# Kernel tuning notes

Hardware: AMD Instinct MI355X
Metric: run time of the kernel (lower is better)

Reference implementation:

```python
import jax, jax.numpy as jnp
import numpy as np

B, S, D, H = 4, 2048, 1024, 16
DH = D // H
NEG = -1e9


def setup_inputs() -> dict:
    key = jax.random.key(0)
    ks = jax.random.split(key, 6)
    return {
        "q_raw": jax.random.normal(ks[0], (B, S, D), jnp.float32),
        "kv_raw": jax.random.normal(ks[1], (B, S, D), jnp.float32),
        "padding_mask": jnp.ones((B, S), jnp.int32),
        "Wq": jax.random.normal(ks[2], (D, D), jnp.float32) * 0.02,
        "Wk": jax.random.normal(ks[3], (D, D), jnp.float32) * 0.02,
        "Wv": jax.random.normal(ks[4], (D, D), jnp.float32) * 0.02,
        "Wo": jax.random.normal(ks[5], (D, D), jnp.float32) * 0.02,
    }


def _split_heads(x):
    # (B, S, D) -> (B, H, S, DH)
    return x.reshape(B, S, H, DH).transpose(0, 2, 1, 3)


def reference(q_raw, kv_raw, padding_mask, Wq, Wk, Wv, Wo):
    # nn.Linear (no bias): y = x @ W.T
    q = _split_heads(q_raw @ Wq.T)
    k = _split_heads(kv_raw @ Wk.T)
    v = _split_heads(kv_raw @ Wv.T)

    scale = 1.0 / jnp.sqrt(jnp.float32(DH))
    scores = jnp.einsum("bhqd,bhkd->bhqk", q, k) * scale  # (B,H,S,S)

    # padding mask: 0 -> masked (broadcast over query dim), as in torch code
    pad = (padding_mask == 0)[:, None, None, :]  # (B,1,1,S)
    scores = jnp.where(pad, NEG, scores)
    # causal mask (only applied when padding_mask given, matching original)
    causal = jnp.triu(jnp.ones((S, S), bool), k=1)  # (S,S)
    scores = jnp.where(causal[None, None], NEG, scores)

    w = jax.nn.softmax(scores, axis=-1)
    att = jnp.einsum("bhqk,bhkd->bhqd", w, v)  # (B,H,S,DH)
    att = att.transpose(0, 2, 1, 3).reshape(B, S, D)
    return att @ Wo.T
```

## Files before the change

kernel.cpp:

```cpp
#include <hip/hip_runtime.h>
#include <stdint.h>

typedef __attribute__((ext_vector_type(8))) short  short8;
typedef __attribute__((ext_vector_type(4))) float  f32x4;
typedef __attribute__((ext_vector_type(4))) unsigned short us4;
typedef __attribute__((ext_vector_type(4))) unsigned int u32x4;

static __device__ __forceinline__ unsigned short f2bf(float x) {
  unsigned u = __builtin_bit_cast(unsigned, x);
  u += 0x7FFFu + ((u >> 16) & 1u);
  return (unsigned short)(u >> 16);
}

static __device__ __forceinline__ unsigned cvt_pk_bf16(float lo, float hi) {
  unsigned r;
  asm("v_cvt_pk_bf16_f32 %0, %1, %2" : "=v"(r) : "v"(lo), "v"(hi));
  return r;
}

__global__ __launch_bounds__(256) void cvt6(const float* __restrict__ q_raw,
                                            const float* __restrict__ kv_raw,
                                            const float* __restrict__ Wq,
                                            const float* __restrict__ Wk,
                                            const float* __restrict__ Wv,
                                            const float* __restrict__ Wo,
                                            unsigned short* __restrict__ qbf,
                                            unsigned short* __restrict__ kvbf,
                                            unsigned short* __restrict__ wbf) {
  const int y = blockIdx.y;
  const float* in;
  unsigned short* out;
  int n4;
  if (y == 0)      { in = q_raw;  out = qbf;  n4 = 2097152; }
  else if (y == 1) { in = kv_raw; out = kvbf; n4 = 2097152; }
  else {
    in  = (y == 2) ? Wq : (y == 3) ? Wk : (y == 4) ? Wv : Wo;
    out = wbf + (size_t)(y - 2) * 1048576;
    n4 = 262144;
  }
  int i = blockIdx.x * 256 + threadIdx.x;
  const int stride = gridDim.x * 256;
  for (; i < n4; i += stride) {
    f32x4 v = *((const f32x4*)in + i);
    us4 o = { f2bf(v[0]), f2bf(v[1]), f2bf(v[2]), f2bf(v[3]) };
    *((us4*)out + i) = o;
  }
}

__global__ __launch_bounds__(1024) void bias_kernel(const int* __restrict__ pm,
                                                    float* __restrict__ bias,
                                                    unsigned* __restrict__ flagmask) {
  __shared__ unsigned m;
  const int b = blockIdx.x, tid = threadIdx.x;
  if (tid == 0) m = 0;
  __syncthreads();
  const int i0 = b * 2048 + tid;
  const int z0 = pm[i0], z1 = pm[i0 + 1024];
  bias[i0]        = z0 ? 0.f : -1.0e9f;
  bias[i0 + 1024] = z1 ? 0.f : -1.0e9f;
  const int wv = tid >> 6;
  unsigned long long b0 = __ballot(z0 == 0);
  unsigned long long b1 = __ballot(z1 == 0);
  if ((tid & 63) == 0) {
    unsigned bits = (b0 ? (1u << wv) : 0u) | (b1 ? (1u << (wv + 16)) : 0u);
    if (bits) atomicOr(&m, bits);
  }
  __syncthreads();
  if (tid == 0) flagmask[b] = m;
}

static __device__ __forceinline__ void g2l16(const void* g, void* l) {
  __builtin_amdgcn_global_load_lds(
      (const __attribute__((address_space(1))) void*)g,
      (__attribute__((address_space(3))) void*)l, 16, 0, 0);
}

__global__ __launch_bounds__(256, 5) void gemm_proj(const unsigned short* __restrict__ qbf,
                                                    const unsigned short* __restrict__ kvbf,
                                                    const unsigned short* __restrict__ wbf,
                                                    unsigned short* __restrict__ Qp,
                                                    unsigned short* __restrict__ Kp,
                                                    unsigned short* __restrict__ Vtp,
                                                    float qscale) {
  __shared__ unsigned short Alds[2][4096];
  __shared__ unsigned short Blds[2][4096];
  const int tid  = threadIdx.x;
  const int lane = tid & 63;
  const int w    = tid >> 6;
  const int g    = lane >> 4;
  const int li   = lane & 15;

  const int l = blockIdx.x;
  const int xcd = l & 7, j = l >> 3;
  const int mstep = j & 7, rn = j >> 3;
  const int region = rn >> 3;
  const int n0 = (rn & 7) * 128;
  const int m0 = (xcd * 8 + mstep) * 128;
  const int wm = (w >> 1) * 64;
  const int wn = (w & 1) * 64;

  const unsigned short* A = (region == 0) ? qbf : kvbf;
  const unsigned short* W = wbf + (size_t)region * 1048576;

  int aoff[4], boff[4];
#pragma unroll
  for (int mi = 0; mi < 4; ++mi) {
    int row = wm + mi * 16 + li;
    aoff[mi] = row * 32 + (g ^ ((row >> 1) & 3)) * 8;
  }
#pragma unroll
  for (int ni = 0; ni < 4; ++ni) {
    int col = wn + ni * 16 + li;
    boff[ni] = col * 32 + (g ^ ((col >> 1) & 3)) * 8;
  }

  const int s1 = tid, s2 = 256 + tid;
  const int r1 = s1 >> 2, gc1 = (s1 & 3) ^ ((r1 >> 1) & 3);
  const int r2 = s2 >> 2, gc2 = (s2 & 3) ^ ((r2 >> 1) & 3);
  const unsigned short* gA1 = A + (size_t)(m0 + r1) * 1024 + gc1 * 8;
  const unsigned short* gA2 = A + (size_t)(m0 + r2) * 1024 + gc2 * 8;
  const unsigned short* gB1 = W + (size_t)(n0 + r1) * 1024 + gc1 * 8;
  const unsigned short* gB2 = W + (size_t)(n0 + r2) * 1024 + gc2 * 8;

  f32x4 acc[4][4] = {};

  g2l16(gA1, &Alds[0][w * 512]); g2l16(gA2, &Alds[0][2048 + w * 512]);
  g2l16(gB1, &Blds[0][w * 512]); g2l16(gB2, &Blds[0][2048 + w * 512]);
  gA1 += 32; gA2 += 32; gB1 += 32; gB2 += 32;

  int cur = 0;
#pragma unroll 1
  for (int kt = 0; kt < 32; ++kt) {
    if (kt < 31) {
      g2l16(gA1, &Alds[cur ^ 1][w * 512]); g2l16(gA2, &Alds[cur ^ 1][2048 + w * 512]);
      g2l16(gB1, &Blds[cur ^ 1][w * 512]); g2l16(gB2, &Blds[cur ^ 1][2048 + w * 512]);
      gA1 += 32; gA2 += 32; gB1 += 32; gB2 += 32;
      asm volatile("s_waitcnt vmcnt(4)" ::: "memory");
    } else {
      asm volatile("s_waitcnt vmcnt(0)" ::: "memory");
    }
    __builtin_amdgcn_s_barrier();
    short8 af[4], bf[4];
#pragma unroll
    for (int mi = 0; mi < 4; ++mi) af[mi] = *(const short8*)&Alds[cur][aoff[mi]];
#pragma unroll
    for (int ni = 0; ni < 4; ++ni) bf[ni] = *(const short8*)&Blds[cur][boff[ni]];
#pragma unroll
    for (int mi = 0; mi < 4; ++mi)
#pragma unroll
      for (int ni = 0; ni < 4; ++ni)
        acc[mi][ni] = __builtin_amdgcn_mfma_f32_16x16x32_bf16(af[mi], bf[ni], acc[mi][ni], 0, 0, 0);
    __builtin_amdgcn_s_barrier();
    cur ^= 1;
  }

  if (region == 2) {
#pragma unroll
    for (int mi = 0; mi < 4; ++mi) {
      int mb = m0 + wm + mi * 16 + g * 4;
      int bb = mb >> 11, s = mb & 2047;
#pragma unroll
      for (int ni = 0; ni < 4; ++ni) {
        int n = n0 + wn + ni * 16 + li;
        us4 pk = { f2bf(acc[mi][ni][0]), f2bf(acc[mi][ni][1]),
                   f2bf(acc[mi][ni][2]), f2bf(acc[mi][ni][3]) };
        *(us4*)&Vtp[(size_t)(bb * 1024 + n) * 2048 + s] = pk;
      }
    }
  } else {
    unsigned short* C = (region == 0) ? Qp : Kp;
    const float sc = (region == 0) ? qscale : 1.0f;
#pragma unroll
    for (int mi = 0; mi < 4; ++mi) {
      int mb = m0 + wm + mi * 16 + g * 4;
#pragma unroll
      for (int ni = 0; ni < 4; ++ni) {
        int n = n0 + wn + ni * 16 + li;
#pragma unroll
        for (int r = 0; r < 4; ++r)
          C[(size_t)(mb + r) * 1024 + n] = f2bf(acc[mi][ni][r] * sc);
      }
    }
  }
}

__global__ __launch_bounds__(256) void gemm_out(const unsigned short* __restrict__ A,
                                                const unsigned short* __restrict__ W,
                                                float* __restrict__ C) {
  __shared__ unsigned short Alds[2][4096];
  __shared__ unsigned short Blds[2][4096];
  const int tid  = threadIdx.x;
  const int lane = tid & 63;
  const int w    = tid >> 6;
  const int g    = lane >> 4;
  const int li   = lane & 15;

  const int l = blockIdx.x;
  const int xcd = l & 7, j = l >> 3;
  const int mstep = j & 7, nt = j >> 3;
  const int m0 = (xcd * 8 + mstep) * 128;
  const int n0 = nt * 128;
  const int wm = (w >> 1) * 64;
  const int wn = (w & 1) * 64;

  int aoff[4], boff[4];
#pragma unroll
  for (int mi = 0; mi < 4; ++mi) {
    int row = wm + mi * 16 + li;
    aoff[mi] = row * 32 + (g ^ ((row >> 1) & 3)) * 8;
  }
#pragma unroll
  for (int ni = 0; ni < 4; ++ni) {
    int col = wn + ni * 16 + li;
    boff[ni] = col * 32 + (g ^ ((col >> 1) & 3)) * 8;
  }

  const int s1 = tid, s2 = 256 + tid;
  const int r1 = s1 >> 2, gc1 = (s1 & 3) ^ ((r1 >> 1) & 3);
  const int r2 = s2 >> 2, gc2 = (s2 & 3) ^ ((r2 >> 1) & 3);
  const unsigned short* gA1 = A + (size_t)(m0 + r1) * 1024 + gc1 * 8;
  const unsigned short* gA2 = A + (size_t)(m0 + r2) * 1024 + gc2 * 8;
  const unsigned short* gB1 = W + (size_t)(n0 + r1) * 1024 + gc1 * 8;
  const unsigned short* gB2 = W + (size_t)(n0 + r2) * 1024 + gc2 * 8;

  f32x4 acc[4][4] = {};

  g2l16(gA1, &Alds[0][w * 512]); g2l16(gA2, &Alds[0][2048 + w * 512]);
  g2l16(gB1, &Blds[0][w * 512]); g2l16(gB2, &Blds[0][2048 + w * 512]);
  gA1 += 32; gA2 += 32; gB1 += 32; gB2 += 32;

  int cur = 0;
#pragma unroll 1
  for (int kt = 0; kt < 32; ++kt) {
    if (kt < 31) {
      g2l16(gA1, &Alds[cur ^ 1][w * 512]); g2l16(gA2, &Alds[cur ^ 1][2048 + w * 512]);
      g2l16(gB1, &Blds[cur ^ 1][w * 512]); g2l16(gB2, &Blds[cur ^ 1][2048 + w * 512]);
      gA1 += 32; gA2 += 32; gB1 += 32; gB2 += 32;
      asm volatile("s_waitcnt vmcnt(4)" ::: "memory");
    } else {
      asm volatile("s_waitcnt vmcnt(0)" ::: "memory");
    }
    __builtin_amdgcn_s_barrier();
    short8 af[4], bf[4];
#pragma unroll
    for (int mi = 0; mi < 4; ++mi) af[mi] = *(const short8*)&Alds[cur][aoff[mi]];
#pragma unroll
    for (int ni = 0; ni < 4; ++ni) bf[ni] = *(const short8*)&Blds[cur][boff[ni]];
#pragma unroll
    for (int mi = 0; mi < 4; ++mi)
#pragma unroll
      for (int ni = 0; ni < 4; ++ni)
        acc[mi][ni] = __builtin_amdgcn_mfma_f32_16x16x32_bf16(af[mi], bf[ni], acc[mi][ni], 0, 0, 0);
    __builtin_amdgcn_s_barrier();
    cur ^= 1;
  }

#pragma unroll
  for (int mi = 0; mi < 4; ++mi) {
    int mb = m0 + wm + mi * 16 + g * 4;
#pragma unroll
    for (int ni = 0; ni < 4; ++ni) {
      int n = n0 + wn + ni * 16 + li;
#pragma unroll
      for (int r = 0; r < 4; ++r)
        C[(size_t)(mb + r) * 1024 + n] = acc[mi][ni][r];
    }
  }
}

__global__ __launch_bounds__(256, 4) void attn_kernel(const unsigned short* __restrict__ Qp,
                                                      const unsigned short* __restrict__ Kp,
                                                      const unsigned short* __restrict__ Vt,
                                                      const float* __restrict__ bias,
                                                      const unsigned* __restrict__ flagmask,
                                                      unsigned short* __restrict__ att) {
  __shared__ unsigned short Klds[2][64 * 64];
  __shared__ unsigned short Vlds[2][64 * 64];

  const int tid = threadIdx.x, lane = tid & 63, w = tid >> 6;
  const int g = lane >> 4, li = lane & 15;

  const int rid = blockIdx.x + (blockIdx.y << 4);
  const int xcd = rid & 7, kk = rid >> 3;
  const int bh = (kk & 7) | (xcd << 3);
  const int b = bh >> 4, h = bh & 15;
  const int tA = kk >> 3, tB = 31 - tA;
  const int nA = tA + 1, nB = tB + 1;

  const unsigned smask = flagmask[b];

  const int s1 = tid, s2 = tid + 256;
  const int r1 = s1 >> 3, c1 = (s1 & 7) ^ (r1 & 7);
  const int r2 = s2 >> 3, c2 = (s2 & 7) ^ (r2 & 7);
  const unsigned short* Kb1 = Kp + (size_t)(b * 2048 + r1) * 1024 + h * 64 + c1 * 8;
  const unsigned short* Kb2 = Kp + (size_t)(b * 2048 + r2) * 1024 + h * 64 + c2 * 8;
  const unsigned short* Vb1 = Vt + (size_t)(b * 1024 + h * 64 + r1) * 2048 + c1 * 8;
  const unsigned short* Vb2 = Vt + (size_t)(b * 1024 + h * 64 + r2) * 2048 + c2 * 8;

  int foffK[2][4], foffV[2][4];
#pragma unroll
  for (int ks = 0; ks < 2; ++ks)
#pragma unroll
    for (int ni = 0; ni < 4; ++ni) {
      const int krow = (ni >> 1) * 32 + (li >> 2) * 8 + (ni & 1) * 4 + (li & 3);
      foffK[ks][ni] = krow * 64 + (((ks * 4 + g) ^ (krow & 7)) * 8);
      const int vrow = ni * 16 + li;
      foffV[ks][ni] = vrow * 64 + (((ks * 4 + g) ^ (vrow & 7)) * 8);
    }

  const float* bbase = bias + b * 2048 + g * 8;

  short8 ones;
#pragma unroll
  for (int j2 = 0; j2 < 8; ++j2) ones[j2] = (short)0x3F80;

  int qw = tA * 64 + w * 16;
  short8 qfr[2];
#pragma unroll
  for (int ks = 0; ks < 2; ++ks)
    qfr[ks] = *(const short8*)&Qp[((size_t)(b * 2048 + qw + li)) * 1024 +
                                  h * 64 + ks * 32 + g * 8];

  f32x4 acco[4] = {};
  f32x4 lacc = {};
  float m = -3.0e38f;
  const f32x4 Z = {0.f, 0.f, 0.f, 0.f};

  auto stage = [&](int kt, int bufn) {
    const size_t ko = (size_t)kt * 65536, vo = (size_t)kt * 64;
    g2l16(Kb1 + ko, &Klds[bufn][w * 512]);
    g2l16(Kb2 + ko, &Klds[bufn][2048 + w * 512]);
    g2l16(Vb1 + vo, &Vlds[bufn][w * 512]);
    g2l16(Vb2 + vo, &Vlds[bufn][2048 + w * 512]);
  };

  auto body = [&](int kt, bool diag, int buf) {
    f32x4 s[4];
    __builtin_amdgcn_s_setprio(1);
#pragma unroll
    for (int ni = 0; ni < 4; ++ni) {
      short8 kf = *(const short8*)&Klds[buf][foffK[0][ni]];
      s[ni] = __builtin_amdgcn_mfma_f32_16x16x32_bf16(kf, qfr[0], Z, 0, 0, 0);
    }
#pragma unroll
    for (int ni = 0; ni < 4; ++ni) {
      short8 kf = *(const short8*)&Klds[buf][foffK[1][ni]];
      s[ni] = __builtin_amdgcn_mfma_f32_16x16x32_bf16(kf, qfr[1], s[ni], 0, 0, 0);
    }
    __builtin_amdgcn_s_setprio(0);
    if ((smask >> kt) & 1u) {
#pragma unroll
      for (int ni = 0; ni < 4; ++ni) {
        f32x4 bv = *(const f32x4*)&bbase[kt * 64 + (ni >> 1) * 32 + (ni & 1) * 4];
#pragma unroll
        for (int r = 0; r < 4; ++r) s[ni][r] += bv[r];
      }
    }
    if (diag) {
      const int q0 = qw + li;
#pragma unroll
      for (int ni = 0; ni < 4; ++ni) {
        const int kb = kt * 64 + (ni >> 1) * 32 + g * 8 + (ni & 1) * 4;
#pragma unroll
        for (int r = 0; r < 4; ++r)
          if (kb + r > q0) s[ni][r] = -1.0e9f;
      }
    }
    f32x4 tv;
#pragma unroll
    for (int r = 0; r < 4; ++r)
      tv[r] = fmaxf(fmaxf(s[0][r], s[1][r]), fmaxf(s[2][r], s[3][r]));
    float tm = fmaxf(fmaxf(tv[0], tv[1]), fmaxf(tv[2], tv[3]));
    tm = fmaxf(tm, __shfl_xor(tm, 16));
    tm = fmaxf(tm, __shfl_xor(tm, 32));
    if (__any(tm > m + 8.0f)) {
      const float mn = fmaxf(m, tm);
      const float al = __builtin_amdgcn_exp2f(m - mn);
      m = mn;
      float alpv[4];
#pragma unroll
      for (int r = 0; r < 4; ++r)
        alpv[r] = __builtin_bit_cast(float,
            __builtin_amdgcn_ds_bpermute((g * 4 + r) * 4, __builtin_bit_cast(int, al)));
#pragma unroll
      for (int r = 0; r < 4; ++r) {
        lacc[r] *= alpv[r];
#pragma unroll
        for (int df = 0; df < 4; ++df) acco[df][r] *= alpv[r];
      }
    }
    unsigned wpk[4][2];
#pragma unroll
    for (int ni = 0; ni < 4; ++ni) {
#pragma unroll
      for (int a2 = 0; a2 < 2; ++a2) {
        float lo = __builtin_amdgcn_exp2f(s[ni][2 * a2]     - m);
        float hi = __builtin_amdgcn_exp2f(s[ni][2 * a2 + 1] - m);
        wpk[ni][a2] = cvt_pk_bf16(lo, hi);
      }
    }
#pragma unroll
    for (int ks = 0; ks < 2; ++ks) {
      u32x4 pw = { wpk[2 * ks][0], wpk[2 * ks][1], wpk[2 * ks + 1][0], wpk[2 * ks + 1][1] };
      const short8 pa = __builtin_bit_cast(short8, pw);
      short8 vf[4];
#pragma unroll
      for (int df = 0; df < 4; ++df) vf[df] = *(const short8*)&Vlds[buf][foffV[ks][df]];
      __builtin_amdgcn_s_setprio(1);
#pragma unroll
      for (int df = 0; df < 4; ++df)
        acco[df] = __builtin_amdgcn_mfma_f32_16x16x32_bf16(pa, vf[df], acco[df], 0, 0, 0);
      lacc = __builtin_amdgcn_mfma_f32_16x16x32_bf16(pa, ones, lacc, 0, 0, 0);
      __builtin_amdgcn_s_setprio(0);
    }
  };

  auto epilogue = [&]() {
    float inv[4];
#pragma unroll
    for (int r = 0; r < 4; ++r) inv[r] = __builtin_amdgcn_rcpf(lacc[r]);
    const int qb0 = qw + g * 4;
#pragma unroll
    for (int df = 0; df < 4; ++df) {
      const int d = h * 64 + df * 16 + li;
#pragma unroll
      for (int r = 0; r < 4; ++r)
        att[(size_t)(b * 2048 + qb0 + r) * 1024 + d] = f2bf(acco[df][r] * inv[r]);
    }
  };

  stage(0, 0);
  int buf = 0;

#pragma unroll 1
  for (int kt = 0; kt < nA; ++kt) {
    stage((kt + 1 < nA) ? kt + 1 : 0, buf ^ 1);
    asm volatile("s_waitcnt vmcnt(4)" ::: "memory");
    __builtin_amdgcn_s_barrier();
    body(kt, kt == nA - 1, buf);
    __builtin_amdgcn_s_barrier();
    buf ^= 1;
  }

  epilogue();
  qw = tB * 64 + w * 16;
#pragma unroll
  for (int ks = 0; ks < 2; ++ks)
    qfr[ks] = *(const short8*)&Qp[((size_t)(b * 2048 + qw + li)) * 1024 +
                                  h * 64 + ks * 32 + g * 8];
#pragma unroll
  for (int df = 0; df < 4; ++df) acco[df] = Z;
  lacc = Z;
  m = -3.0e38f;

#pragma unroll 1
  for (int kt = 0; kt < nB; ++kt) {
    if (kt + 1 < nB) {
      stage(kt + 1, buf ^ 1);
      asm volatile("s_waitcnt vmcnt(4)" ::: "memory");
    } else {
      asm volatile("s_waitcnt vmcnt(0)" ::: "memory");
    }
    __builtin_amdgcn_s_barrier();
    body(kt, kt == nB - 1, buf);
    __builtin_amdgcn_s_barrier();
    buf ^= 1;
  }

  epilogue();
}

extern "C" void kernel_launch(void* const* d_in, const int* in_sizes, int n_in,
                              void* d_out, int out_size, void* d_ws, size_t ws_size,
                              hipStream_t stream) {
  const float* q_raw  = (const float*)d_in[0];
  const float* kv_raw = (const float*)d_in[1];
  const int*   pmask  = (const int*)d_in[2];
  const float* Wq = (const float*)d_in[3];
  const float* Wk = (const float*)d_in[4];
  const float* Wv = (const float*)d_in[5];
  const float* Wo = (const float*)d_in[6];
  float* out = (float*)d_out;

  const size_t NEL = 8388608;
  const size_t WEL = 1048576;
  unsigned short* ws   = (unsigned short*)d_ws;
  unsigned short* qbf  = ws;
  unsigned short* kvbf = qbf + NEL;
  unsigned short* wbf  = kvbf + NEL;
  unsigned short* Qp   = wbf + 4 * WEL;
  unsigned short* Kp   = Qp + NEL;
  unsigned short* Vtp  = Kp + NEL;
  float*          bias = (float*)(Vtp + NEL);
  unsigned*       flagmask = (unsigned*)(bias + 8192);
  unsigned short* att  = qbf;

  const float sc = 0.125f * 1.44269504088896340736f;

  cvt6<<<dim3(512, 6), 256, 0, stream>>>(q_raw, kv_raw, Wq, Wk, Wv, Wo, qbf, kvbf, wbf);
  bias_kernel<<<4, 1024, 0, stream>>>(pmask, bias, flagmask);
  gemm_proj<<<1536, 256, 0, stream>>>(qbf, kvbf, wbf, Qp, Kp, Vtp, sc);
  attn_kernel<<<dim3(16, 64), 256, 0, stream>>>(Qp, Kp, Vtp, bias, flagmask, att);
  gemm_out<<<512, 256, 0, stream>>>(att, wbf + 3 * WEL, out);
}
```

Measured before the change: 199.2 us.

## Fuse fp32-to-bf16 activation conversion into projection GEMM A-tile loads

Activations are no longer converted to bf16 in a separate pass. The projection GEMM now reads fp32 q_raw/kv_raw directly into registers, converts them with v_cvt_pk_bf16, and writes them into the swizzled LDS tile after the MFMAs, while the weight tiles still use direct global-to-LDS loads. This removes a full read and write of the bf16 activation copies. In exchange the A operand is loaded twice as many bytes per tile, goes through registers with more VGPR pressure (the occupancy hint of 5 is dropped), and relies on __syncthreads instead of the explicit vmcnt waits.

Result: faster. 181.5 us (-8.9%).

```diff
diff --git a/kernel.cpp b/kernel.cpp
--- a/kernel.cpp
+++ b/kernel.cpp
@@ -18,29 +18,17 @@
   return r;
 }
 
-__global__ __launch_bounds__(256) void cvt6(const float* __restrict__ q_raw,
-                                            const float* __restrict__ kv_raw,
-                                            const float* __restrict__ Wq,
+__global__ __launch_bounds__(256) void cvtW(const float* __restrict__ Wq,
                                             const float* __restrict__ Wk,
                                             const float* __restrict__ Wv,
                                             const float* __restrict__ Wo,
-                                            unsigned short* __restrict__ qbf,
-                                            unsigned short* __restrict__ kvbf,
                                             unsigned short* __restrict__ wbf) {
   const int y = blockIdx.y;
-  const float* in;
-  unsigned short* out;
-  int n4;
-  if (y == 0)      { in = q_raw;  out = qbf;  n4 = 2097152; }
-  else if (y == 1) { in = kv_raw; out = kvbf; n4 = 2097152; }
-  else {
-    in  = (y == 2) ? Wq : (y == 3) ? Wk : (y == 4) ? Wv : Wo;
-    out = wbf + (size_t)(y - 2) * 1048576;
-    n4 = 262144;
-  }
+  const float* in = (y == 0) ? Wq : (y == 1) ? Wk : (y == 2) ? Wv : Wo;
+  unsigned short* out = wbf + (size_t)y * 1048576;
   int i = blockIdx.x * 256 + threadIdx.x;
   const int stride = gridDim.x * 256;
-  for (; i < n4; i += stride) {
+  for (; i < 262144; i += stride) {
     f32x4 v = *((const f32x4*)in + i);
     us4 o = { f2bf(v[0]), f2bf(v[1]), f2bf(v[2]), f2bf(v[3]) };
     *((us4*)out + i) = o;
@@ -75,13 +63,13 @@
       (__attribute__((address_space(3))) void*)l, 16, 0, 0);
 }
 
-__global__ __launch_bounds__(256, 5) void gemm_proj(const unsigned short* __restrict__ qbf,
-                                                    const unsigned short* __restrict__ kvbf,
-                                                    const unsigned short* __restrict__ wbf,
-                                                    unsigned short* __restrict__ Qp,
-                                                    unsigned short* __restrict__ Kp,
-                                                    unsigned short* __restrict__ Vtp,
-                                                    float qscale) {
+__global__ __launch_bounds__(256) void gemm_proj(const float* __restrict__ q_raw,
+                                                 const float* __restrict__ kv_raw,
+                                                 const unsigned short* __restrict__ wbf,
+                                                 unsigned short* __restrict__ Qp,
+                                                 unsigned short* __restrict__ Kp,
+                                                 unsigned short* __restrict__ Vtp,
+                                                 float qscale) {
   __shared__ unsigned short Alds[2][4096];
   __shared__ unsigned short Blds[2][4096];
   const int tid  = threadIdx.x;
@@ -99,7 +87,7 @@
   const int wm = (w >> 1) * 64;
   const int wn = (w & 1) * 64;
 
-  const unsigned short* A = (region == 0) ? qbf : kvbf;
+  const float* Araw = (region == 0) ? q_raw : kv_raw;
   const unsigned short* W = wbf + (size_t)region * 1048576;
 
   int aoff[4], boff[4];
@@ -117,29 +105,40 @@
   const int s1 = tid, s2 = 256 + tid;
   const int r1 = s1 >> 2, gc1 = (s1 & 3) ^ ((r1 >> 1) & 3);
   const int r2 = s2 >> 2, gc2 = (s2 & 3) ^ ((r2 >> 1) & 3);
-  const unsigned short* gA1 = A + (size_t)(m0 + r1) * 1024 + gc1 * 8;
-  const unsigned short* gA2 = A + (size_t)(m0 + r2) * 1024 + gc2 * 8;
+  const float* fA1 = Araw + (size_t)(m0 + r1) * 1024 + gc1 * 8;
+  const float* fA2 = Araw + (size_t)(m0 + r2) * 1024 + gc2 * 8;
   const unsigned short* gB1 = W + (size_t)(n0 + r1) * 1024 + gc1 * 8;
   const unsigned short* gB2 = W + (size_t)(n0 + r2) * 1024 + gc2 * 8;
 
   f32x4 acc[4][4] = {};
 
-  g2l16(gA1, &Alds[0][w * 512]); g2l16(gA2, &Alds[0][2048 + w * 512]);
-  g2l16(gB1, &Blds[0][w * 512]); g2l16(gB2, &Blds[0][2048 + w * 512]);
-  gA1 += 32; gA2 += 32; gB1 += 32; gB2 += 32;
+  {
+    f32x4 a0 = *(const f32x4*)fA1, a1 = *(const f32x4*)(fA1 + 4);
+    f32x4 b0 = *(const f32x4*)fA2, b1 = *(const f32x4*)(fA2 + 4);
+    fA1 += 32; fA2 += 32;
+    g2l16(gB1, &Blds[0][w * 512]); g2l16(gB2, &Blds[0][2048 + w * 512]);
+    gB1 += 32; gB2 += 32;
+    u32x4 w1 = { cvt_pk_bf16(a0[0], a0[1]), cvt_pk_bf16(a0[2], a0[3]),
+                 cvt_pk_bf16(a1[0], a1[1]), cvt_pk_bf16(a1[2], a1[3]) };
+    u32x4 w2 = { cvt_pk_bf16(b0[0], b0[1]), cvt_pk_bf16(b0[2], b0[3]),
+                 cvt_pk_bf16(b1[0], b1[1]), cvt_pk_bf16(b1[2], b1[3]) };
+    *(u32x4*)&Alds[0][s1 * 8] = w1;
+    *(u32x4*)&Alds[0][s2 * 8] = w2;
+  }
+  __syncthreads();
 
   int cur = 0;
 #pragma unroll 1
   for (int kt = 0; kt < 32; ++kt) {
-    if (kt < 31) {
-      g2l16(gA1, &Alds[cur ^ 1][w * 512]); g2l16(gA2, &Alds[cur ^ 1][2048 + w * 512]);
+    f32x4 a0, a1, b0, b1;
+    const bool pf = (kt < 31);
+    if (pf) {
+      a0 = *(const f32x4*)fA1; a1 = *(const f32x4*)(fA1 + 4);
+      b0 = *(const f32x4*)fA2; b1 = *(const f32x4*)(fA2 + 4);
+      fA1 += 32; fA2 += 32;
       g2l16(gB1, &Blds[cur ^ 1][w * 512]); g2l16(gB2, &Blds[cur ^ 1][2048 + w * 512]);
-      gA1 += 32; gA2 += 32; gB1 += 32; gB2 += 32;
-      asm volatile("s_waitcnt vmcnt(4)" ::: "memory");
-    } else {
-      asm volatile("s_waitcnt vmcnt(0)" ::: "memory");
-    }
-    __builtin_amdgcn_s_barrier();
+      gB1 += 32; gB2 += 32;
+    }
     short8 af[4], bf[4];
 #pragma unroll
     for (int mi = 0; mi < 4; ++mi) af[mi] = *(const short8*)&Alds[cur][aoff[mi]];
@@ -150,7 +149,15 @@
 #pragma unroll
       for (int ni = 0; ni < 4; ++ni)
         acc[mi][ni] = __builtin_amdgcn_mfma_f32_16x16x32_bf16(af[mi], bf[ni], acc[mi][ni], 0, 0, 0);
-    __builtin_amdgcn_s_barrier();
+    if (pf) {
+      u32x4 w1 = { cvt_pk_bf16(a0[0], a0[1]), cvt_pk_bf16(a0[2], a0[3]),
+                   cvt_pk_bf16(a1[0], a1[1]), cvt_pk_bf16(a1[2], a1[3]) };
+      u32x4 w2 = { cvt_pk_bf16(b0[0], b0[1]), cvt_pk_bf16(b0[2], b0[3]),
+                   cvt_pk_bf16(b1[0], b1[1]), cvt_pk_bf16(b1[2], b1[3]) };
+      *(u32x4*)&Alds[cur ^ 1][s1 * 8] = w1;
+      *(u32x4*)&Alds[cur ^ 1][s2 * 8] = w2;
+    }
+    __syncthreads();
     cur ^= 1;
   }
 
@@ -485,21 +492,19 @@
   const size_t NEL = 8388608;
   const size_t WEL = 1048576;
   unsigned short* ws   = (unsigned short*)d_ws;
-  unsigned short* qbf  = ws;
-  unsigned short* kvbf = qbf + NEL;
-  unsigned short* wbf  = kvbf + NEL;
+  unsigned short* att  = ws;
+  unsigned short* wbf  = att + NEL;
   unsigned short* Qp   = wbf + 4 * WEL;
   unsigned short* Kp   = Qp + NEL;
   unsigned short* Vtp  = Kp + NEL;
   float*          bias = (float*)(Vtp + NEL);
   unsigned*       flagmask = (unsigned*)(bias + 8192);
-  unsigned short* att  = qbf;
 
   const float sc = 0.125f * 1.44269504088896340736f;
 
-  cvt6<<<dim3(512, 6), 256, 0, stream>>>(q_raw, kv_raw, Wq, Wk, Wv, Wo, qbf, kvbf, wbf);
+  cvtW<<<dim3(256, 4), 256, 0, stream>>>(Wq, Wk, Wv, Wo, wbf);
   bias_kernel<<<4, 1024, 0, stream>>>(pmask, bias, flagmask);
-  gemm_proj<<<1536, 256, 0, stream>>>(qbf, kvbf, wbf, Qp, Kp, Vtp, sc);
+  gemm_proj<<<1536, 256, 0, stream>>>(q_raw, kv_raw, wbf, Qp, Kp, Vtp, sc);
   attn_kernel<<<dim3(16, 64), 256, 0, stream>>>(Qp, Kp, Vtp, bias, flagmask, att);
   gemm_out<<<512, 256, 0, stream>>>(att, wbf + 3 * WEL, out);
 }
```
